# Kernel optimization log

Hardware: AMD Instinct MI355X
Metric: run time of the kernel (lower is better)

Reference implementation:

```python
import jax, jax.numpy as jnp
import numpy as np

N_NODES = 50000
E_EDGES = 800000
NEG_SLOPE = 0.2  # PyG GATConv LeakyReLU slope
BN_EPS = 1e-5


def _gat(x, src, dst, W, a_s, a_d, b, heads, ch, concat):
    """One GATConv (PyG semantics, eval mode): gather, per-edge attention,
    segment softmax over destination neighborhoods, scatter-add aggregation."""
    n = x.shape[0]
    h = (x @ W).reshape(n, heads, ch)                      # [N,H,C]
    es = jnp.sum(h * a_s, axis=-1)                         # [N,H] alpha_src per node
    ed = jnp.sum(h * a_d, axis=-1)                         # [N,H] alpha_dst per node
    e = jax.nn.leaky_relu(es[src] + ed[dst], NEG_SLOPE)    # [E,H] edge logits
    m = jax.ops.segment_max(e, dst, num_segments=n)        # stable segment softmax
    ex = jnp.exp(e - m[dst])
    den = jax.ops.segment_sum(ex, dst, num_segments=n)
    alpha = ex / den[dst]                                  # [E,H]
    out = jax.ops.segment_sum(h[src] * alpha[:, :, None], dst, num_segments=n)  # [N,H,C]
    out = out.reshape(n, heads * ch) if concat else out.mean(axis=1)
    return out + b


def _bn(x, g, b):
    # eval-mode BatchNorm1d with running_mean=0, running_var=1
    return x * (g / jnp.sqrt(1.0 + BN_EPS)) + b


def setup_inputs() -> dict:
    key = jax.random.key(0)
    k = jax.random.split(key, 24)
    s = 0.1
    inp = {
        "x": jax.random.normal(k[0], (N_NODES, 9), jnp.float32),
        "edge_index": jax.random.randint(k[1], (2, E_EDGES), 0, N_NODES, jnp.int32),
        "W1": jax.random.normal(k[2], (9, 512), jnp.float32) * s,
        "a1s": jax.random.normal(k[3], (8, 64), jnp.float32) * s,
        "a1d": jax.random.normal(k[4], (8, 64), jnp.float32) * s,
        "b1": jax.random.normal(k[5], (512,), jnp.float32) * s,
        "W2": jax.random.normal(k[6], (512, 128), jnp.float32) * s,
        "a2s": jax.random.normal(k[7], (4, 32), jnp.float32) * s,
        "a2d": jax.random.normal(k[8], (4, 32), jnp.float32) * s,
        "b2": jax.random.normal(k[9], (128,), jnp.float32) * s,
        "W3": jax.random.normal(k[10], (128, 32), jnp.float32) * s,
        "a3s": jax.random.normal(k[11], (1, 32), jnp.float32) * s,
        "a3d": jax.random.normal(k[12], (1, 32), jnp.float32) * s,
        "b3": jax.random.normal(k[13], (32,), jnp.float32) * s,
        "g1": jax.random.uniform(k[14], (512,), jnp.float32, 0.5, 1.5),
        "be1": jax.random.normal(k[15], (512,), jnp.float32) * s,
        "g2": jax.random.uniform(k[16], (128,), jnp.float32, 0.5, 1.5),
        "be2": jax.random.normal(k[17], (128,), jnp.float32) * s,
        "g3": jax.random.uniform(k[18], (32,), jnp.float32, 0.5, 1.5),
        "be3": jax.random.normal(k[19], (32,), jnp.float32) * s,
        "Wh": jax.random.normal(k[20], (32, 1), jnp.float32) * s,
        "bh": jax.random.normal(k[21], (1,), jnp.float32) * s,
    }
    return inp


def reference(x, edge_index, W1, a1s, a1d, b1, W2, a2s, a2d, b2,
              W3, a3s, a3d, b3, g1, be1, g2, be2, g3, be3, Wh, bh):
    n = x.shape[0]
    loops = jnp.arange(n, dtype=edge_index.dtype)          # PyG add_self_loops=True
    src = jnp.concatenate([edge_index[0], loops])
    dst = jnp.concatenate([edge_index[1], loops])
    h = _gat(x, src, dst, W1, a1s, a1d, b1, heads=8, ch=64, concat=True)
    h = jax.nn.elu(_bn(h, g1, be1))
    h = _gat(h, src, dst, W2, a2s, a2d, b2, heads=4, ch=32, concat=True)
    h = jax.nn.elu(_bn(h, g2, be2))
    h = _gat(h, src, dst, W3, a3s, a3d, b3, heads=1, ch=32, concat=False)
    h = jax.nn.elu(_bn(h, g3, be3))
    return h @ Wh + bh                                     # [N,1]
```

## Files before the change

kernel.cpp:

```cpp
#include <hip/hip_runtime.h>
#include <hip/hip_bf16.h>
#include <math.h>

#define N_NODES 50000
#define E_EDGES 800000
#define ET (E_EDGES + N_NODES)
#define NBLK_SCAN ((N_NODES + 255) / 256)
#define MPAD 50048
#define NPB_T1 16
#define WROWS 160

typedef __attribute__((ext_vector_type(4))) float f32x4;
typedef __attribute__((ext_vector_type(8))) _Float16 half8;
typedef __attribute__((ext_vector_type(2))) _Float16 half2v;


__global__ void zero_int_kernel(int* __restrict__ p, int n) {
    int i = blockIdx.x * blockDim.x + threadIdx.x;
    if (i < n) p[i] = 0;
}

__global__ void hist_kernel(const int* __restrict__ ei, int* __restrict__ cnt) {
    int e = blockIdx.x * blockDim.x + threadIdx.x;
    if (e < ET) {
        int d = (e < E_EDGES) ? ei[E_EDGES + e] : (e - E_EDGES);
        atomicAdd(&cnt[d], 1);
    }
}

__global__ void scan1_kernel(const int* __restrict__ cnt, int* __restrict__ rp,
                             int* __restrict__ bsum) {
    __shared__ int s[256];
    int i = blockIdx.x * 256 + threadIdx.x;
    int v = (i < N_NODES) ? cnt[i] : 0;
    s[threadIdx.x] = v;
    __syncthreads();
    for (int off = 1; off < 256; off <<= 1) {
        int t = (threadIdx.x >= off) ? s[threadIdx.x - off] : 0;
        __syncthreads();
        s[threadIdx.x] += t;
        __syncthreads();
    }
    if (i < N_NODES) rp[i + 1] = s[threadIdx.x];
    if (threadIdx.x == 255) bsum[blockIdx.x] = s[255];
}

__global__ void scan2_kernel(int* __restrict__ bsum, int nb) {
    __shared__ int s[256];
    int v = (threadIdx.x < nb) ? bsum[threadIdx.x] : 0;
    s[threadIdx.x] = v;
    __syncthreads();
    for (int off = 1; off < 256; off <<= 1) {
        int t = (threadIdx.x >= off) ? s[threadIdx.x - off] : 0;
        __syncthreads();
        s[threadIdx.x] += t;
        __syncthreads();
    }
    if (threadIdx.x < nb) bsum[threadIdx.x] = (threadIdx.x == 0) ? 0 : s[threadIdx.x - 1];
}

__global__ void scan3_kernel(int* __restrict__ rp, const int* __restrict__ bsum,
                             int* __restrict__ cursor) {
    int i = blockIdx.x * 256 + threadIdx.x;
    if (i == 0) rp[0] = 0;
    if (i < N_NODES) {
        int incl = rp[i + 1] + bsum[i >> 8];
        rp[i + 1] = incl;
        cursor[i] = incl - cursor[i];
    }
}

__global__ void fill_kernel(const int* __restrict__ ei, int* __restrict__ cursor,
                            int* __restrict__ col) {
    int e = blockIdx.x * blockDim.x + threadIdx.x;
    if (e < ET) {
        int s_, d;
        if (e < E_EDGES) { s_ = ei[e]; d = ei[E_EDGES + e]; }
        else             { s_ = e - E_EDGES; d = s_; }
        int p = atomicAdd(&cursor[d], 1);
        col[p] = s_;
    }
}


__global__ __launch_bounds__(256) void es_ed1_kernel(const float* __restrict__ x,
        const float* __restrict__ W1, const float* __restrict__ a1s,
        const float* __restrict__ a1d,
        float* __restrict__ es, float* __restrict__ ed) {
    __shared__ float sM[144];
    int tid = threadIdx.x;
    if (tid < 144) {
        int which = tid / 72, idx = tid % 72, k = idx / 8, h = idx % 8;
        const float* a = which ? a1d : a1s;
        float s = 0.f;
        for (int c = 0; c < 64; c++) s += W1[k * 512 + h * 64 + c] * a[h * 64 + c];
        sM[tid] = s;
    }
    __syncthreads();
    int n = blockIdx.x * 256 + tid;
    if (n >= N_NODES) return;
    float xr[9];
#pragma unroll
    for (int k = 0; k < 9; k++) xr[k] = x[(size_t)n * 9 + k];
#pragma unroll
    for (int h = 0; h < 8; h++) {
        float s1 = 0.f, s2 = 0.f;
#pragma unroll
        for (int k = 0; k < 9; k++) {
            s1 += xr[k] * sM[k * 8 + h];
            s2 += xr[k] * sM[72 + k * 8 + h];
        }
        es[(size_t)n * 8 + h] = s1;
        ed[(size_t)n * 8 + h] = s2;
    }
}

__global__ __launch_bounds__(128) void agg1_kernel(const float* __restrict__ x,
        const int* __restrict__ rp, const int* __restrict__ col,
        const float* __restrict__ es, const float* __restrict__ ed,
        float* __restrict__ aggx) {
    __shared__ int   s_src[64];
    __shared__ float s_x[64][9];
    __shared__ float s_es[64][12];
    __shared__ float s_w[64][9];
    __shared__ float s_m[8], s_den[8], s_scale[8], s_ed[8];
    int n = blockIdx.x, tid = threadIdx.x;
    int start = rp[n], end = rp[n + 1];
    if (tid < 8) { s_m[tid] = -INFINITY; s_den[tid] = 0.f; s_ed[tid] = ed[(size_t)n * 8 + tid]; }
    __syncthreads();
    int ghh = tid >> 4, glane = tid & 15;
    int hh = tid / 9, k = tid - hh * 9;
    float p0 = 0.f, p1 = 0.f, p2 = 0.f, p3 = 0.f;
    for (int cs = start; cs < end; cs += 64) {
        int cnt = min(64, end - cs);
        if (tid < cnt) s_src[tid] = col[cs + tid];
        __syncthreads();
        for (int q = tid; q < cnt * 9; q += 128) {
            int e = q / 9, kk = q - e * 9;
            s_x[e][kk] = x[(size_t)s_src[e] * 9 + kk];
        }
        for (int q = tid; q < cnt * 2; q += 128) {
            int e = q >> 1, h4 = (q & 1) * 4;
            *(float4*)&s_es[e][h4] = *(const float4*)&es[(size_t)s_src[e] * 8 + h4];
        }
        __syncthreads();
        float lmax = -INFINITY;
        for (int e = glane; e < cnt; e += 16) {
            float l = s_es[e][ghh] + s_ed[ghh];
            l = (l > 0.f) ? l : 0.2f * l;
            s_w[e][ghh] = l;
            lmax = fmaxf(lmax, l);
        }
#pragma unroll
        for (int off = 8; off > 0; off >>= 1) lmax = fmaxf(lmax, __shfl_xor(lmax, off));
        float mold = s_m[ghh];
        float nm = fmaxf(mold, lmax);
        float fac = __expf(mold - nm);
        float psum = 0.f;
        for (int e = glane; e < cnt; e += 16) {
            float w = __expf(s_w[e][ghh] - nm);
            s_w[e][ghh] = w;
            psum += w;
        }
#pragma unroll
        for (int off = 8; off > 0; off >>= 1) psum += __shfl_xor(psum, off);
        if (glane == 0) { s_den[ghh] = s_den[ghh] * fac + psum; s_m[ghh] = nm; s_scale[ghh] = fac; }
        __syncthreads();
        if (tid < 72) {
            float fac2 = s_scale[hh];
            p0 *= fac2; p1 *= fac2; p2 *= fac2; p3 *= fac2;
            int e = 0;
            for (; e + 4 <= cnt; e += 4) {
                p0 += s_w[e][hh]     * s_x[e][k];
                p1 += s_w[e + 1][hh] * s_x[e + 1][k];
                p2 += s_w[e + 2][hh] * s_x[e + 2][k];
                p3 += s_w[e + 3][hh] * s_x[e + 3][k];
            }
            for (; e < cnt; e++) p0 += s_w[e][hh] * s_x[e][k];
        }
        __syncthreads();
    }
    if (tid < 72) {
        aggx[(size_t)n * 72 + tid] = (p0 + p1 + p2 + p3) / s_den[hh];
    }
}

__global__ __launch_bounds__(256) void transform1_kernel(const float* __restrict__ aggx,
        const float* __restrict__ W1, const float* __restrict__ b1,
        const float* __restrict__ g1, const float* __restrict__ be1,
        _Float16* __restrict__ Af) {
    __shared__ float s_a[NPB_T1 * 72];
    int tid = threadIdx.x;
    int n0 = blockIdx.x * NPB_T1;
    int nn = min(NPB_T1, N_NODES - n0);
    for (int q = tid; q < nn * 72; q += 256) s_a[q] = aggx[(size_t)n0 * 72 + q];
    int c0 = tid * 2;
    int hh = c0 >> 6;
    float2 wv[9];
#pragma unroll
    for (int k = 0; k < 9; k++) wv[k] = *(const float2*)&W1[k * 512 + c0];
    float2 bv = *(const float2*)&b1[c0];
    float2 gv = *(const float2*)&g1[c0];
    float2 ev = *(const float2*)&be1[c0];
    float gs0 = gv.x / sqrtf(1.00001f), gs1 = gv.y / sqrtf(1.00001f);
    __syncthreads();
    for (int i = 0; i < nn; i++) {
        const float* ar = &s_a[i * 72 + hh * 9];
        float v0 = bv.x, v1 = bv.y;
#pragma unroll
        for (int k = 0; k < 9; k++) { float a = ar[k]; v0 += a * wv[k].x; v1 += a * wv[k].y; }
        v0 = v0 * gs0 + ev.x;
        v1 = v1 * gs1 + ev.y;
        v0 = (v0 > 0.f) ? v0 : expm1f(v0);
        v1 = (v1 > 0.f) ? v1 : expm1f(v1);
        half2v hp;
        hp[0] = (_Float16)v0;
        hp[1] = (_Float16)v1;
        *(half2v*)&Af[(size_t)(n0 + i) * 512 + c0] = hp;
    }
}

__global__ void prep2_kernel(const float* __restrict__ W2,
                             const float* __restrict__ a2s, const float* __restrict__ a2d,
                             _Float16* __restrict__ WT) {
    int t = blockIdx.x * 256 + threadIdx.x;
    if (t < 65536) {
        int k = t >> 7, c = t & 127;
        WT[(size_t)c * 512 + k] = (_Float16)W2[t];
    } else if (t < 65536 + 4096) {
        int q = t - 65536;
        int hd8 = q >> 9, k = q & 511;
        const float* a = (hd8 < 4) ? a2s : a2d;
        int hd = hd8 & 3;
        float s = 0.f;
#pragma unroll
        for (int c = 0; c < 32; c++) s += W2[k * 128 + hd * 32 + c] * a[hd * 32 + c];
        WT[(size_t)(128 + hd8) * 512 + k] = (_Float16)s;
    }
}


__global__ __launch_bounds__(256) void gemm2_mfma_kernel(
        const _Float16* __restrict__ A, const _Float16* __restrict__ WT,
        _Float16* __restrict__ h2, float* __restrict__ es, float* __restrict__ ed) {
    __shared__ _Float16 ldsA[128 * 64];
    __shared__ _Float16 ldsW[WROWS * 64];
    int tid = threadIdx.x;
    int wv = tid >> 6;
    int lane = tid & 63;
    int lrow = lane & 15, kgrp = lane >> 4;
    int m0 = blockIdx.x * 128;

    f32x4 acc[2][9];
#pragma unroll
    for (int m = 0; m < 2; m++)
#pragma unroll
        for (int n = 0; n < 9; n++) acc[m][n] = (f32x4){0.f, 0.f, 0.f, 0.f};

    for (int kk = 0; kk < 512; kk += 64) {
#pragma unroll
        for (int i = 0; i < 4; i++) {
            int gid = tid + 256 * i;
            int row = gid >> 3, kg = gid & 7;
            half8 v = *(const half8*)(A + (size_t)(m0 + row) * 512 + kk + kg * 8);
            *(half8*)(ldsA + row * 64 + ((kg ^ (row & 7)) << 3)) = v;
        }
#pragma unroll
        for (int i = 0; i < 5; i++) {
            int gid = tid + 256 * i;
            int row = gid >> 3, kg = gid & 7;
            half8 v = *(const half8*)(WT + (size_t)row * 512 + kk + kg * 8);
            *(half8*)(ldsW + row * 64 + ((kg ^ (row & 7)) << 3)) = v;
        }
        __syncthreads();
#pragma unroll
        for (int ks = 0; ks < 2; ks++) {
            int kg = ks * 4 + kgrp;
            half8 af[2];
#pragma unroll
            for (int m = 0; m < 2; m++) {
                int row = wv * 32 + m * 16 + lrow;
                af[m] = *(const half8*)(ldsA + row * 64 + ((kg ^ (row & 7)) << 3));
            }
#pragma unroll
            for (int n = 0; n < 9; n++) {
                int colr = n * 16 + lrow;
                half8 wf = *(const half8*)(ldsW + colr * 64 + ((kg ^ (colr & 7)) << 3));
#pragma unroll
                for (int m = 0; m < 2; m++)
                    acc[m][n] = __builtin_amdgcn_mfma_f32_16x16x32_f16(af[m], wf, acc[m][n], 0, 0, 0);
            }
        }
        __syncthreads();
    }
#pragma unroll
    for (int m = 0; m < 2; m++) {
#pragma unroll
        for (int r = 0; r < 4; r++) {
            int row = m0 + wv * 32 + m * 16 + (lane >> 4) * 4 + r;
            if (row < N_NODES) {
#pragma unroll
                for (int n = 0; n < 8; n++)
                    h2[(size_t)row * 128 + n * 16 + lrow] = (_Float16)acc[m][n][r];
                if (lrow < 4)      es[(size_t)row * 4 + lrow]     = acc[m][8][r];
                else if (lrow < 8) ed[(size_t)row * 4 + lrow - 4] = acc[m][8][r];
            }
        }
    }
}


__global__ __launch_bounds__(64) void agg2_fused_kernel(
        const _Float16* __restrict__ hin,
        const int* __restrict__ rp, const int* __restrict__ col,
        const float* __restrict__ es, const float* __restrict__ ed,
        const float* __restrict__ b2, const float* __restrict__ g2,
        const float* __restrict__ be2,
        const float* __restrict__ W3, const float* __restrict__ a3s,
        const float* __restrict__ a3d,
        _Float16* __restrict__ h3, float* __restrict__ es3, float* __restrict__ ed3) {
    constexpr int H = 4, HC = 128, LPH = 16, G = 4, CH = 64;
    __shared__ int   s_src[CH];
    __shared__ float s_w[H][CH];
    __shared__ float s_red[G][HC];
    __shared__ float s_res[HC];
    __shared__ float s_m[H], s_den[H], s_scale[H], s_ed[H];

    int n = blockIdx.x, tid = threadIdx.x;
    int start = rp[n], end = rp[n + 1];
    if (tid < H) { s_m[tid] = -INFINITY; s_den[tid] = 0.f; s_ed[tid] = ed[(size_t)n * H + tid]; }
    __syncthreads();

    int ghh = tid >> 4, glane = tid & 15;
    int g = tid >> 4, rl = tid & 15;
    int hh2 = rl >> 2;
    float a0[8], a1[8];
#pragma unroll
    for (int j = 0; j < 8; j++) { a0[j] = 0.f; a1[j] = 0.f; }

    for (int cs = start; cs < end; cs += CH) {
        int cnt = min(CH, end - cs);
        if (tid < cnt) s_src[tid] = col[cs + tid];
        __syncthreads();

        {
            float lmax = -INFINITY;
            for (int e = glane; e < cnt; e += LPH) {
                float l = es[(size_t)s_src[e] * H + ghh] + s_ed[ghh];
                l = (l > 0.f) ? l : 0.2f * l;
                s_w[ghh][e] = l;
                lmax = fmaxf(lmax, l);
            }
#pragma unroll
            for (int off = 8; off > 0; off >>= 1) lmax = fmaxf(lmax, __shfl_xor(lmax, off));
            float mold = s_m[ghh];
            float nm = fmaxf(mold, lmax);
            float fac = __expf(mold - nm);
            float psum = 0.f;
            for (int e = glane; e < cnt; e += LPH) {
                float w = __expf(s_w[ghh][e] - nm);
                s_w[ghh][e] = w;
                psum += w;
            }
#pragma unroll
            for (int off = 8; off > 0; off >>= 1) psum += __shfl_xor(psum, off);
            if (glane == 0) { s_den[ghh] = s_den[ghh] * fac + psum; s_m[ghh] = nm; s_scale[ghh] = fac; }
        }
        __syncthreads();

        {
            float fac = s_scale[hh2];
#pragma unroll
            for (int j = 0; j < 8; j++) a0[j] *= fac;
            int e = g;
            for (; e + G < cnt; e += 2 * G) {
                float w0 = s_w[hh2][e];
                float w1 = s_w[hh2][e + G];
                half8 v0 = *(const half8*)&hin[(size_t)s_src[e] * HC + rl * 8];
                half8 v1 = *(const half8*)&hin[(size_t)s_src[e + G] * HC + rl * 8];
#pragma unroll
                for (int j = 0; j < 8; j++) a0[j] += w0 * (float)v0[j];
#pragma unroll
                for (int j = 0; j < 8; j++) a1[j] += w1 * (float)v1[j];
            }
            if (e < cnt) {
                float w0 = s_w[hh2][e];
                half8 v0 = *(const half8*)&hin[(size_t)s_src[e] * HC + rl * 8];
#pragma unroll
                for (int j = 0; j < 8; j++) a0[j] += w0 * (float)v0[j];
            }
        }
        __syncthreads();
    }

#pragma unroll
    for (int j = 0; j < 8; j++) s_red[g][rl * 8 + j] = a0[j] + a1[j];
    __syncthreads();

    const float rsq = 0.99999499f;
#pragma unroll
    for (int half = 0; half < 2; half++) {
        int c = tid + half * 64;
        float r = s_red[0][c] + s_red[1][c] + s_red[2][c] + s_red[3][c];
        r /= s_den[c >> 5];
        r += b2[c];
        r = r * (g2[c] * rsq) + be2[c];
        r = (r > 0.f) ? r : expm1f(r);
        s_res[c] = r;
    }
    __syncthreads();

    int halfk = tid >> 5, j = tid & 31;
    float v = 0.f;
#pragma unroll 16
    for (int c = halfk * 64; c < halfk * 64 + 64; c++) v += s_res[c] * W3[c * 32 + j];
    v += __shfl_xor(v, 32);
    if (tid < 32) h3[(size_t)n * 32 + j] = (_Float16)v;
    float p1 = v * a3s[j], p2 = v * a3d[j];
#pragma unroll
    for (int off = 16; off > 0; off >>= 1) {
        p1 += __shfl_xor(p1, off);
        p2 += __shfl_xor(p2, off);
    }
    if (tid == 0) { es3[n] = p1; ed3[n] = p2; }
}


__global__ __launch_bounds__(64) void agg3_fused_kernel(
        const _Float16* __restrict__ hin,
        const int* __restrict__ rp, const int* __restrict__ col,
        const float* __restrict__ es3, const float* __restrict__ ed3,
        const float* __restrict__ b3, const float* __restrict__ g3,
        const float* __restrict__ be3,
        const float* __restrict__ Wh, const float* __restrict__ bh,
        float* __restrict__ out) {
    constexpr int G = 16, CH = 64;
    __shared__ int   s_src[CH];
    __shared__ float s_w[CH];
    __shared__ float s_red[G][36];
    __shared__ float s_m1, s_den1, s_scale1, s_ed1;

    int n = blockIdx.x, tid = threadIdx.x;
    int start = rp[n], end = rp[n + 1];
    if (tid == 0) { s_m1 = -INFINITY; s_den1 = 0.f; s_ed1 = ed3[n]; }
    __syncthreads();

    int g = tid >> 2, rl = tid & 3;
    float a0[8], a1[8];
#pragma unroll
    for (int j = 0; j < 8; j++) { a0[j] = 0.f; a1[j] = 0.f; }

    for (int cs = start; cs < end; cs += CH) {
        int cnt = min(CH, end - cs);
        if (tid < cnt) s_src[tid] = col[cs + tid];
        __syncthreads();

        float lmax = -INFINITY;
        float l = 0.f;
        if (tid < cnt) {
            l = es3[s_src[tid]] + s_ed1;
            l = (l > 0.f) ? l : 0.2f * l;
            lmax = l;
        }
#pragma unroll
        for (int off = 32; off > 0; off >>= 1) lmax = fmaxf(lmax, __shfl_xor(lmax, off));
        float mold = s_m1;
        float nm = fmaxf(mold, lmax);
        float fac = __expf(mold - nm);
        float w = 0.f;
        if (tid < cnt) {
            w = __expf(l - nm);
            s_w[tid] = w;
        }
        float psum = w;
#pragma unroll
        for (int off = 32; off > 0; off >>= 1) psum += __shfl_xor(psum, off);
        if (tid == 0) { s_den1 = s_den1 * fac + psum; s_m1 = nm; s_scale1 = fac; }
        __syncthreads();

        {
#pragma unroll
            for (int j = 0; j < 8; j++) a0[j] *= fac;
            int e = g;
            for (; e + G < cnt; e += 2 * G) {
                float w0 = s_w[e];
                float w1 = s_w[e + G];
                half8 v0 = *(const half8*)&hin[(size_t)s_src[e] * 32 + rl * 8];
                half8 v1 = *(const half8*)&hin[(size_t)s_src[e + G] * 32 + rl * 8];
#pragma unroll
                for (int j = 0; j < 8; j++) a0[j] += w0 * (float)v0[j];
#pragma unroll
                for (int j = 0; j < 8; j++) a1[j] += w1 * (float)v1[j];
            }
            if (e < cnt) {
                float w0 = s_w[e];
                half8 v0 = *(const half8*)&hin[(size_t)s_src[e] * 32 + rl * 8];
#pragma unroll
                for (int j = 0; j < 8; j++) a0[j] += w0 * (float)v0[j];
            }
        }
        __syncthreads();
    }

#pragma unroll
    for (int j = 0; j < 8; j++) s_red[g][rl * 8 + j] = a0[j] + a1[j];
    __syncthreads();

    const float rsq = 0.99999499f;
    float p = 0.f;
    if (tid < 32) {
        float r = 0.f;
#pragma unroll
        for (int q = 0; q < G; q++) r += s_red[q][tid];
        r /= s_den1;
        r += b3[tid];
        r = r * (g3[tid] * rsq) + be3[tid];
        r = (r > 0.f) ? r : expm1f(r);
        p = r * Wh[tid];
    }
#pragma unroll
    for (int off = 16; off > 0; off >>= 1) p += __shfl_xor(p, off);
    if (tid == 0) out[n] = p + bh[0];
}


extern "C" void kernel_launch(void* const* d_in, const int* in_sizes, int n_in,
                              void* d_out, int out_size, void* d_ws, size_t ws_size,
                              hipStream_t stream) {
    const float* x   = (const float*)d_in[0];
    const int*   ei  = (const int*)d_in[1];
    const float* W1  = (const float*)d_in[2];
    const float* a1s = (const float*)d_in[3];
    const float* a1d = (const float*)d_in[4];
    const float* b1  = (const float*)d_in[5];
    const float* W2  = (const float*)d_in[6];
    const float* a2s = (const float*)d_in[7];
    const float* a2d = (const float*)d_in[8];
    const float* b2  = (const float*)d_in[9];
    const float* W3  = (const float*)d_in[10];
    const float* a3s = (const float*)d_in[11];
    const float* a3d = (const float*)d_in[12];
    const float* b3  = (const float*)d_in[13];
    const float* g1  = (const float*)d_in[14];
    const float* be1 = (const float*)d_in[15];
    const float* g2  = (const float*)d_in[16];
    const float* be2 = (const float*)d_in[17];
    const float* g3  = (const float*)d_in[18];
    const float* be3 = (const float*)d_in[19];
    const float* Wh  = (const float*)d_in[20];
    const float* bh  = (const float*)d_in[21];
    float* out = (float*)d_out;

    char* ws = (char*)d_ws;
    size_t off = 0;
    auto alloc = [&](size_t bytes) -> void* {
        void* p = ws + off;
        off += (bytes + 255) & ~(size_t)255;
        return p;
    };
    int*   row_ptr = (int*)alloc((N_NODES + 1) * sizeof(int));
    int*   cursor  = (int*)alloc((N_NODES + 1) * sizeof(int));
    int*   bsum    = (int*)alloc(256 * sizeof(int));
    int*   col_src = (int*)alloc((size_t)ET * sizeof(int));
    float* es      = (float*)alloc((size_t)N_NODES * 8 * sizeof(float));
    float* ed      = (float*)alloc((size_t)N_NODES * 8 * sizeof(float));
    float* es3     = (float*)alloc((size_t)N_NODES * sizeof(float));
    float* ed3     = (float*)alloc((size_t)N_NODES * sizeof(float));
    float* aggx    = (float*)alloc((size_t)N_NODES * 72 * sizeof(float));
    _Float16* h2h  = (_Float16*)alloc((size_t)N_NODES * 128 * sizeof(_Float16));
    _Float16* h3h  = (_Float16*)alloc((size_t)N_NODES * 32 * sizeof(_Float16));
    _Float16* Af   = (_Float16*)alloc((size_t)MPAD * 512 * sizeof(_Float16));
    _Float16* WT   = (_Float16*)alloc((size_t)WROWS * 512 * sizeof(_Float16));

    zero_int_kernel<<<(N_NODES + 1 + 255) / 256, 256, 0, stream>>>(cursor, N_NODES + 1);
    hist_kernel<<<(ET + 255) / 256, 256, 0, stream>>>(ei, cursor);
    scan1_kernel<<<NBLK_SCAN, 256, 0, stream>>>(cursor, row_ptr, bsum);
    scan2_kernel<<<1, 256, 0, stream>>>(bsum, NBLK_SCAN);
    scan3_kernel<<<NBLK_SCAN, 256, 0, stream>>>(row_ptr, bsum, cursor);
    fill_kernel<<<(ET + 255) / 256, 256, 0, stream>>>(ei, cursor, col_src);

    es_ed1_kernel<<<(N_NODES + 255) / 256, 256, 0, stream>>>(x, W1, a1s, a1d, es, ed);
    agg1_kernel<<<N_NODES, 128, 0, stream>>>(x, row_ptr, col_src, es, ed, aggx);
    transform1_kernel<<<(N_NODES + NPB_T1 - 1) / NPB_T1, 256, 0, stream>>>(aggx, W1, b1, g1, be1, Af);

    prep2_kernel<<<288, 256, 0, stream>>>(W2, a2s, a2d, WT);
    gemm2_mfma_kernel<<<MPAD / 128, 256, 0, stream>>>(Af, WT, h2h, es, ed);
    agg2_fused_kernel<<<N_NODES, 64, 0, stream>>>(h2h, row_ptr, col_src, es, ed,
                                                  b2, g2, be2, W3, a3s, a3d,
                                                  h3h, es3, ed3);

    agg3_fused_kernel<<<N_NODES, 64, 0, stream>>>(h3h, row_ptr, col_src, es3, ed3,
                                                  b3, g3, be3, Wh, bh, out);
}
```

Baseline: 374.0 us.

## Fuse layer-1 transform into GEMM2 prologue and merge prep kernels

The layer-1 linear, batch-norm and ELU transform now runs inside the GEMM2 kernel, which computes each 64-wide K slice of fp16 activations straight into LDS from the staged aggregated features. This removes the large fp16 intermediate Af and its global write and read. The es/ed layer-1 prep and the W2 prep kernels are merged into one launch, and the zero kernel becomes hipMemsetAsync. The cost is extra per-block ALU work and LDS use in the GEMM, which may lower occupancy. aggx is padded to MPAD so the tail block can read it; those extra rows are never written, so the padded output rows come from uninitialized data.

```diff
diff --git a/kernel.cpp b/kernel.cpp
--- a/kernel.cpp
+++ b/kernel.cpp
@@ -7,18 +7,13 @@
 #define ET (E_EDGES + N_NODES)
 #define NBLK_SCAN ((N_NODES + 255) / 256)
 #define MPAD 50048
-#define NPB_T1 16
 #define WROWS 160
+#define PREP2_BLKS 288
 
 typedef __attribute__((ext_vector_type(4))) float f32x4;
 typedef __attribute__((ext_vector_type(8))) _Float16 half8;
-typedef __attribute__((ext_vector_type(2))) _Float16 half2v;
-
-
-__global__ void zero_int_kernel(int* __restrict__ p, int n) {
-    int i = blockIdx.x * blockDim.x + threadIdx.x;
-    if (i < n) p[i] = 0;
-}
+typedef __attribute__((ext_vector_type(4))) _Float16 half4v;
+
 
 __global__ void hist_kernel(const int* __restrict__ ei, int* __restrict__ cnt) {
     int e = blockIdx.x * blockDim.x + threadIdx.x;
@@ -83,37 +78,57 @@
 }
 
 
-__global__ __launch_bounds__(256) void es_ed1_kernel(const float* __restrict__ x,
-        const float* __restrict__ W1, const float* __restrict__ a1s,
-        const float* __restrict__ a1d,
-        float* __restrict__ es, float* __restrict__ ed) {
-    __shared__ float sM[144];
-    int tid = threadIdx.x;
-    if (tid < 144) {
-        int which = tid / 72, idx = tid % 72, k = idx / 8, h = idx % 8;
-        const float* a = which ? a1d : a1s;
-        float s = 0.f;
-        for (int c = 0; c < 64; c++) s += W1[k * 512 + h * 64 + c] * a[h * 64 + c];
-        sM[tid] = s;
-    }
-    __syncthreads();
-    int n = blockIdx.x * 256 + tid;
-    if (n >= N_NODES) return;
-    float xr[9];
-#pragma unroll
-    for (int k = 0; k < 9; k++) xr[k] = x[(size_t)n * 9 + k];
-#pragma unroll
-    for (int h = 0; h < 8; h++) {
-        float s1 = 0.f, s2 = 0.f;
-#pragma unroll
-        for (int k = 0; k < 9; k++) {
-            s1 += xr[k] * sM[k * 8 + h];
-            s2 += xr[k] * sM[72 + k * 8 + h];
-        }
-        es[(size_t)n * 8 + h] = s1;
-        ed[(size_t)n * 8 + h] = s2;
-    }
-}
+__global__ __launch_bounds__(256) void prep_fused_kernel(
+        const float* __restrict__ x, const float* __restrict__ W1,
+        const float* __restrict__ a1s, const float* __restrict__ a1d,
+        float* __restrict__ es, float* __restrict__ ed,
+        const float* __restrict__ W2, const float* __restrict__ a2s,
+        const float* __restrict__ a2d, _Float16* __restrict__ WT) {
+    int blk = blockIdx.x, tid = threadIdx.x;
+    if (blk < NBLK_SCAN) {
+        __shared__ float sM[144];
+        if (tid < 144) {
+            int which = tid / 72, idx = tid % 72, k = idx / 8, h = idx % 8;
+            const float* a = which ? a1d : a1s;
+            float s = 0.f;
+            for (int c = 0; c < 64; c++) s += W1[k * 512 + h * 64 + c] * a[h * 64 + c];
+            sM[tid] = s;
+        }
+        __syncthreads();
+        int n = blk * 256 + tid;
+        if (n >= N_NODES) return;
+        float xr[9];
+#pragma unroll
+        for (int k = 0; k < 9; k++) xr[k] = x[(size_t)n * 9 + k];
+#pragma unroll
+        for (int h = 0; h < 8; h++) {
+            float s1 = 0.f, s2 = 0.f;
+#pragma unroll
+            for (int k = 0; k < 9; k++) {
+                s1 += xr[k] * sM[k * 8 + h];
+                s2 += xr[k] * sM[72 + k * 8 + h];
+            }
+            es[(size_t)n * 8 + h] = s1;
+            ed[(size_t)n * 8 + h] = s2;
+        }
+    } else {
+        int t = (blk - NBLK_SCAN) * 256 + tid;
+        if (t < 65536) {
+            int k = t >> 7, c = t & 127;
+            WT[(size_t)c * 512 + k] = (_Float16)W2[t];
+        } else if (t < 65536 + 4096) {
+            int q = t - 65536;
+            int hd8 = q >> 9, k = q & 511;
+            const float* a = (hd8 < 4) ? a2s : a2d;
+            int hd = hd8 & 3;
+            float s = 0.f;
+#pragma unroll
+            for (int c = 0; c < 32; c++) s += W2[k * 128 + hd * 32 + c] * a[hd * 32 + c];
+            WT[(size_t)(128 + hd8) * 512 + k] = (_Float16)s;
+        }
+    }
+}
+
 
 __global__ __launch_bounds__(128) void agg1_kernel(const float* __restrict__ x,
         const int* __restrict__ rp, const int* __restrict__ col,
@@ -185,86 +200,39 @@
     }
 }
 
-__global__ __launch_bounds__(256) void transform1_kernel(const float* __restrict__ aggx,
+
+__global__ __launch_bounds__(256) void gemm2_fused_kernel(
+        const float* __restrict__ aggx,
         const float* __restrict__ W1, const float* __restrict__ b1,
         const float* __restrict__ g1, const float* __restrict__ be1,
-        _Float16* __restrict__ Af) {
-    __shared__ float s_a[NPB_T1 * 72];
-    int tid = threadIdx.x;
-    int n0 = blockIdx.x * NPB_T1;
-    int nn = min(NPB_T1, N_NODES - n0);
-    for (int q = tid; q < nn * 72; q += 256) s_a[q] = aggx[(size_t)n0 * 72 + q];
-    int c0 = tid * 2;
-    int hh = c0 >> 6;
-    float2 wv[9];
-#pragma unroll
-    for (int k = 0; k < 9; k++) wv[k] = *(const float2*)&W1[k * 512 + c0];
-    float2 bv = *(const float2*)&b1[c0];
-    float2 gv = *(const float2*)&g1[c0];
-    float2 ev = *(const float2*)&be1[c0];
-    float gs0 = gv.x / sqrtf(1.00001f), gs1 = gv.y / sqrtf(1.00001f);
-    __syncthreads();
-    for (int i = 0; i < nn; i++) {
-        const float* ar = &s_a[i * 72 + hh * 9];
-        float v0 = bv.x, v1 = bv.y;
-#pragma unroll
-        for (int k = 0; k < 9; k++) { float a = ar[k]; v0 += a * wv[k].x; v1 += a * wv[k].y; }
-        v0 = v0 * gs0 + ev.x;
-        v1 = v1 * gs1 + ev.y;
-        v0 = (v0 > 0.f) ? v0 : expm1f(v0);
-        v1 = (v1 > 0.f) ? v1 : expm1f(v1);
-        half2v hp;
-        hp[0] = (_Float16)v0;
-        hp[1] = (_Float16)v1;
-        *(half2v*)&Af[(size_t)(n0 + i) * 512 + c0] = hp;
-    }
-}
-
-__global__ void prep2_kernel(const float* __restrict__ W2,
-                             const float* __restrict__ a2s, const float* __restrict__ a2d,
-                             _Float16* __restrict__ WT) {
-    int t = blockIdx.x * 256 + threadIdx.x;
-    if (t < 65536) {
-        int k = t >> 7, c = t & 127;
-        WT[(size_t)c * 512 + k] = (_Float16)W2[t];
-    } else if (t < 65536 + 4096) {
-        int q = t - 65536;
-        int hd8 = q >> 9, k = q & 511;
-        const float* a = (hd8 < 4) ? a2s : a2d;
-        int hd = hd8 & 3;
-        float s = 0.f;
-#pragma unroll
-        for (int c = 0; c < 32; c++) s += W2[k * 128 + hd * 32 + c] * a[hd * 32 + c];
-        WT[(size_t)(128 + hd8) * 512 + k] = (_Float16)s;
-    }
-}
-
-
-__global__ __launch_bounds__(256) void gemm2_mfma_kernel(
-        const _Float16* __restrict__ A, const _Float16* __restrict__ WT,
+        const _Float16* __restrict__ WT,
         _Float16* __restrict__ h2, float* __restrict__ es, float* __restrict__ ed) {
     __shared__ _Float16 ldsA[128 * 64];
     __shared__ _Float16 ldsW[WROWS * 64];
+    __shared__ float    ldsAgg[128 * 73];
     int tid = threadIdx.x;
     int wv = tid >> 6;
     int lane = tid & 63;
     int lrow = lane & 15, kgrp = lane >> 4;
     int m0 = blockIdx.x * 128;
 
+    for (int q = tid; q < 128 * 72; q += 256) {
+        int row = q / 72, k = q - row * 72;
+        ldsAgg[row * 73 + k] = aggx[(size_t)(m0 + row) * 72 + k];
+    }
+    __syncthreads();
+
     f32x4 acc[2][9];
 #pragma unroll
     for (int m = 0; m < 2; m++)
 #pragma unroll
         for (int n = 0; n < 9; n++) acc[m][n] = (f32x4){0.f, 0.f, 0.f, 0.f};
 
-    for (int kk = 0; kk < 512; kk += 64) {
-#pragma unroll
-        for (int i = 0; i < 4; i++) {
-            int gid = tid + 256 * i;
-            int row = gid >> 3, kg = gid & 7;
-            half8 v = *(const half8*)(A + (size_t)(m0 + row) * 512 + kk + kg * 8);
-            *(half8*)(ldsA + row * 64 + ((kg ^ (row & 7)) << 3)) = v;
-        }
+    int cg = tid & 15, rg = tid >> 4;
+    const float rsq = 0.99999499f;
+
+    for (int step = 0; step < 8; step++) {
+        int kk = step * 64;
 #pragma unroll
         for (int i = 0; i < 5; i++) {
             int gid = tid + 256 * i;
@@ -272,20 +240,51 @@
             half8 v = *(const half8*)(WT + (size_t)row * 512 + kk + kg * 8);
             *(half8*)(ldsW + row * 64 + ((kg ^ (row & 7)) << 3)) = v;
         }
+        int ch0 = kk + cg * 4;
+        float4 w4[9];
+#pragma unroll
+        for (int k = 0; k < 9; k++) w4[k] = *(const float4*)&W1[k * 512 + ch0];
+        float4 bv = *(const float4*)&b1[ch0];
+        float4 gv = *(const float4*)&g1[ch0];
+        float4 ev = *(const float4*)&be1[ch0];
+        float gs0 = gv.x * rsq, gs1 = gv.y * rsq, gs2 = gv.z * rsq, gs3 = gv.w * rsq;
+        int kg = cg >> 1, coff = (cg & 1) * 4;
+#pragma unroll
+        for (int r8 = 0; r8 < 8; r8++) {
+            int row = rg + r8 * 16;
+            const float* ar = &ldsAgg[row * 73 + step * 9];
+            float v0 = bv.x, v1 = bv.y, v2 = bv.z, v3 = bv.w;
+#pragma unroll
+            for (int k = 0; k < 9; k++) {
+                float a = ar[k];
+                v0 += a * w4[k].x; v1 += a * w4[k].y;
+                v2 += a * w4[k].z; v3 += a * w4[k].w;
+            }
+            v0 = v0 * gs0 + ev.x; v1 = v1 * gs1 + ev.y;
+            v2 = v2 * gs2 + ev.z; v3 = v3 * gs3 + ev.w;
+            v0 = (v0 > 0.f) ? v0 : expm1f(v0);
+            v1 = (v1 > 0.f) ? v1 : expm1f(v1);
+            v2 = (v2 > 0.f) ? v2 : expm1f(v2);
+            v3 = (v3 > 0.f) ? v3 : expm1f(v3);
+            half4v hp;
+            hp[0] = (_Float16)v0; hp[1] = (_Float16)v1;
+            hp[2] = (_Float16)v2; hp[3] = (_Float16)v3;
+            *(half4v*)(ldsA + row * 64 + ((kg ^ (row & 7)) << 3) + coff) = hp;
+        }
         __syncthreads();
 #pragma unroll
         for (int ks = 0; ks < 2; ks++) {
-            int kg = ks * 4 + kgrp;
+            int kg2 = ks * 4 + kgrp;
             half8 af[2];
 #pragma unroll
             for (int m = 0; m < 2; m++) {
                 int row = wv * 32 + m * 16 + lrow;
-                af[m] = *(const half8*)(ldsA + row * 64 + ((kg ^ (row & 7)) << 3));
+                af[m] = *(const half8*)(ldsA + row * 64 + ((kg2 ^ (row & 7)) << 3));
             }
 #pragma unroll
             for (int n = 0; n < 9; n++) {
                 int colr = n * 16 + lrow;
-                half8 wf = *(const half8*)(ldsW + colr * 64 + ((kg ^ (colr & 7)) << 3));
+                half8 wf = *(const half8*)(ldsW + colr * 64 + ((kg2 ^ (colr & 7)) << 3));
 #pragma unroll
                 for (int m = 0; m < 2; m++)
                     acc[m][n] = __builtin_amdgcn_mfma_f32_16x16x32_f16(af[m], wf, acc[m][n], 0, 0, 0);
@@ -566,25 +565,25 @@
     float* ed      = (float*)alloc((size_t)N_NODES * 8 * sizeof(float));
     float* es3     = (float*)alloc((size_t)N_NODES * sizeof(float));
     float* ed3     = (float*)alloc((size_t)N_NODES * sizeof(float));
-    float* aggx    = (float*)alloc((size_t)N_NODES * 72 * sizeof(float));
+    float* aggx    = (float*)alloc((size_t)MPAD * 72 * sizeof(float));
     _Float16* h2h  = (_Float16*)alloc((size_t)N_NODES * 128 * sizeof(_Float16));
     _Float16* h3h  = (_Float16*)alloc((size_t)N_NODES * 32 * sizeof(_Float16));
-    _Float16* Af   = (_Float16*)alloc((size_t)MPAD * 512 * sizeof(_Float16));
     _Float16* WT   = (_Float16*)alloc((size_t)WROWS * 512 * sizeof(_Float16));
 
-    zero_int_kernel<<<(N_NODES + 1 + 255) / 256, 256, 0, stream>>>(cursor, N_NODES + 1);
+    hipMemsetAsync(cursor, 0, (N_NODES + 1) * sizeof(int), stream);
     hist_kernel<<<(ET + 255) / 256, 256, 0, stream>>>(ei, cursor);
     scan1_kernel<<<NBLK_SCAN, 256, 0, stream>>>(cursor, row_ptr, bsum);
     scan2_kernel<<<1, 256, 0, stream>>>(bsum, NBLK_SCAN);
     scan3_kernel<<<NBLK_SCAN, 256, 0, stream>>>(row_ptr, bsum, cursor);
     fill_kernel<<<(ET + 255) / 256, 256, 0, stream>>>(ei, cursor, col_src);
 
-    es_ed1_kernel<<<(N_NODES + 255) / 256, 256, 0, stream>>>(x, W1, a1s, a1d, es, ed);
+    prep_fused_kernel<<<NBLK_SCAN + PREP2_BLKS, 256, 0, stream>>>(
+        x, W1, a1s, a1d, es, ed, W2, a2s, a2d, WT);
+
     agg1_kernel<<<N_NODES, 128, 0, stream>>>(x, row_ptr, col_src, es, ed, aggx);
-    transform1_kernel<<<(N_NODES + NPB_T1 - 1) / NPB_T1, 256, 0, stream>>>(aggx, W1, b1, g1, be1, Af);
-
-    prep2_kernel<<<288, 256, 0, stream>>>(W2, a2s, a2d, WT);
-    gemm2_mfma_kernel<<<MPAD / 128, 256, 0, stream>>>(Af, WT, h2h, es, ed);
+
+    gemm2_fused_kernel<<<MPAD / 128, 256, 0, stream>>>(aggx, W1, b1, g1, be1, WT,
+                                                       h2h, es, ed);
     agg2_fused_kernel<<<N_NODES, 64, 0, stream>>>(h2h, row_ptr, col_src, es, ed,
                                                   b2, g2, be2, W3, a3s, a3d,
                                                   h3h, es3, ed3);
```

Measured after the change: 387.1 us. +3.5%, slower.
